# Kernel optimization log

Measured on AMD Instinct MI355X. Metric: run time of the kernel, lower is better.

## Reference

```python
import jax, jax.numpy as jnp
import numpy as np

B, S, DIM = 64, 256, 512
H = 16
DH = DIM // H          # 32
W = 256                # window_size == seq_len
ROPE_BASE = 10000.0


def _rope(x):
    # x: (B, S, H, DH), interleaved-pair RoPE
    pos = jnp.arange(S, dtype=jnp.float32)
    inv_freq = 1.0 / (ROPE_BASE ** (jnp.arange(0, DH, 2, dtype=jnp.float32) / DH))
    sinusoid = pos[:, None] * inv_freq[None, :]            # (S, DH/2)
    sin = jnp.sin(sinusoid)[None, :, None, :]              # (1, S, 1, DH/2)
    cos = jnp.cos(sinusoid)[None, :, None, :]
    x1 = x[..., 0::2]
    x2 = x[..., 1::2]
    r1 = x1 * cos - x2 * sin
    r2 = x1 * sin + x2 * cos
    return jnp.stack([r1, r2], axis=-1).reshape(x.shape)


def setup_inputs() -> dict:
    key = jax.random.key(0)
    ks = jax.random.split(key, 8)
    s = 1.0 / np.sqrt(DIM)
    return {
        "hidden_states": jax.random.normal(ks[0], (B, S, DIM), jnp.float32),
        "Wq": jax.random.normal(ks[1], (DIM, DIM), jnp.float32) * s,
        "bq": jnp.zeros((DIM,), jnp.float32),
        "Wk": jax.random.normal(ks[2], (DIM, DIM), jnp.float32) * s,
        "bk": jnp.zeros((DIM,), jnp.float32),
        "Wv": jax.random.normal(ks[3], (DIM, DIM), jnp.float32) * s,
        "bv": jnp.zeros((DIM,), jnp.float32),
        "bias_table": jax.random.normal(ks[4], (2 * W - 1, H), jnp.float32) * 0.02,
    }


def reference(hidden_states, Wq, bq, Wk, bk, Wv, bv, bias_table):
    b, s, _ = hidden_states.shape
    q = hidden_states @ Wq + bq
    k = hidden_states @ Wk + bk
    v = hidden_states @ Wv + bv
    # (B, S, H, DH)
    q = _rope(q.reshape(b, s, H, DH))
    k = _rope(k.reshape(b, s, H, DH))
    v = v.reshape(b, s, H, DH)
    # (B, H, S, DH)
    q = q.transpose(0, 2, 1, 3)
    k = k.transpose(0, 2, 1, 3)
    v = v.transpose(0, 2, 1, 3)
    scores = jnp.einsum('bhqd,bhkd->bhqk', q, k) / np.sqrt(DH)
    # relative_position_index[i, j] == (i - j) + W - 1
    rel_idx = jnp.arange(W)[:, None] - jnp.arange(W)[None, :] + (W - 1)
    rel_bias = bias_table[rel_idx]                 # (W, W, H)
    rel_bias = rel_bias.transpose(2, 0, 1)[None]   # (1, H, W, W)
    # NOTE: bias added AFTER softmax, faithful to the original module
    probs = jax.nn.softmax(scores, axis=-1) + rel_bias
    ctx = jnp.einsum('bhqk,bhkd->bhqd', probs, v)
    ctx = ctx.transpose(0, 2, 1, 3).reshape(b, s, DIM)
    return ctx
```

## Files before the change

kernel.cpp:

```cpp
#include <hip/hip_runtime.h>
#include <stdint.h>

typedef __attribute__((ext_vector_type(8))) short bf16x8;
typedef __attribute__((ext_vector_type(4))) float f32x4;
typedef __attribute__((ext_vector_type(4))) unsigned int u32x4;

#define MFMA16(a, b, c) __builtin_amdgcn_mfma_f32_16x16x32_bf16(a, b, c, 0, 0, 0)

__device__ __forceinline__ float bf2f(unsigned short u) {
    union { unsigned int i; float f; } x; x.i = ((unsigned int)u) << 16; return x.f;
}
__device__ __forceinline__ unsigned short f2bf(float f) {
    union { float f; unsigned int i; } x; x.f = f;
    unsigned int u = x.i;
    return (unsigned short)((u + 0x7FFFu + ((u >> 16) & 1u)) >> 16);
}

__global__ __launch_bounds__(256) void k_cvt(const float4* __restrict__ in,
                                             unsigned short* __restrict__ out) {
    int i = blockIdx.x * 256 + threadIdx.x;
    float4 v = in[i];
    ushort4 o;
    o.x = f2bf(v.x); o.y = f2bf(v.y); o.z = f2bf(v.z); o.w = f2bf(v.w);
    *(ushort4*)(out + (size_t)i * 4) = o;
}

__global__ __launch_bounds__(256) void k_wt(const float* __restrict__ W0,
                                            const float* __restrict__ W1,
                                            const float* __restrict__ W2,
                                            unsigned short* __restrict__ Wt) {
    __shared__ float t[64][65];
    const float* Wm = (blockIdx.z == 0) ? W0 : (blockIdx.z == 1) ? W1 : W2;
    int k0 = blockIdx.x * 64, n0 = blockIdx.y * 64;
    for (int it = 0; it < 16; ++it) {
        int idx = threadIdx.x + it * 256;
        int r = idx >> 6, c = idx & 63;
        t[r][c] = Wm[(k0 + r) * 512 + n0 + c];
    }
    __syncthreads();
    unsigned short* dst = Wt + (size_t)blockIdx.z * 512 * 512;
    for (int it = 0; it < 16; ++it) {
        int idx = threadIdx.x + it * 256;
        int nr = idx >> 6, kc = idx & 63;
        dst[(n0 + nr) * 512 + k0 + kc] = f2bf(t[kc][nr]);
    }
}

__global__ __launch_bounds__(256) void k_sc(float* __restrict__ cs2) {
    int s = threadIdx.x;
    for (int f = 0; f < 16; ++f) {
        float inv = powf(10000.0f, -(float)f / 16.0f);
        float a = (float)s * inv;
        cs2[(s * 16 + f) * 2 + 0] = cosf(a);
        cs2[(s * 16 + f) * 2 + 1] = sinf(a);
    }
}

__global__ __launch_bounds__(256, 2) void k_gemm(
    const unsigned short* __restrict__ A,
    const unsigned short* __restrict__ Bw,
    const float* __restrict__ bq, const float* __restrict__ bk, const float* __restrict__ bv,
    const float* __restrict__ cs2,
    unsigned short* __restrict__ Qo, unsigned short* __restrict__ Ko, unsigned short* __restrict__ Vo) {
    __shared__ unsigned short a_l[128 * 64];
    __shared__ unsigned short b_l[128 * 64];
    const int tid = threadIdx.x;
    const int wave = tid >> 6, lane = tid & 63;
    const int l15 = lane & 15, l4 = lane >> 4;
    int bid = blockIdx.x;
    int swz = (bid & 7) * 192 + (bid >> 3);
    const int m0 = (swz / 12) * 128;
    const int n0 = (swz % 12) * 128;
    const int wm = (wave >> 1) * 64, wn = (wave & 1) * 64;
    const bool isV = (n0 >= 1024);

    f32x4 zero4 = {0.f, 0.f, 0.f, 0.f};
    f32x4 acc[4][4];
#pragma unroll
    for (int i = 0; i < 4; ++i)
#pragma unroll
        for (int j = 0; j < 4; ++j) acc[i][j] = zero4;

    const int srow = tid >> 3;
    const int skc = (tid & 7) * 8;
    const unsigned short* ga = A + (size_t)(m0 + srow) * 512 + skc;
    const unsigned short* gb = Bw + (size_t)(n0 + srow) * 512 + skc;
    unsigned short* la = a_l + wave * 512;
    unsigned short* lb = b_l + wave * 512;

    for (int kt = 0; kt < 8; ++kt) {
        const unsigned short* pa = ga + kt * 64;
        const unsigned short* pb = gb + kt * 64;
#pragma unroll
        for (int it = 0; it < 4; ++it) {
            __builtin_amdgcn_global_load_lds(
                (const __attribute__((address_space(1))) unsigned int*)(pa + it * (32 * 512)),
                (__attribute__((address_space(3))) unsigned int*)(la + it * 2048), 16, 0, 0);
            __builtin_amdgcn_global_load_lds(
                (const __attribute__((address_space(1))) unsigned int*)(pb + it * (32 * 512)),
                (__attribute__((address_space(3))) unsigned int*)(lb + it * 2048), 16, 0, 0);
        }
        __syncthreads();
#pragma unroll
        for (int kc = 0; kc < 2; ++kc) {
            bf16x8 af[4], bfr[4];
#pragma unroll
            for (int i = 0; i < 4; ++i)
                af[i] = *(const bf16x8*)&a_l[(wm + i * 16 + l15) * 64 + kc * 32 + l4 * 8];
#pragma unroll
            for (int j = 0; j < 4; ++j)
                bfr[j] = *(const bf16x8*)&b_l[(wn + j * 16 + l15) * 64 + kc * 32 + l4 * 8];
            if (!isV) {
#pragma unroll
                for (int i = 0; i < 4; ++i)
#pragma unroll
                    for (int j = 0; j < 4; ++j) acc[i][j] = MFMA16(af[i], bfr[j], acc[i][j]);
            } else {
#pragma unroll
                for (int i = 0; i < 4; ++i)
#pragma unroll
                    for (int j = 0; j < 4; ++j) acc[i][j] = MFMA16(bfr[j], af[i], acc[i][j]);
            }
        }
        __syncthreads();
    }

    if (!isV) {
        const int mat = n0 >> 9;
        unsigned short* __restrict__ dst = (mat == 0) ? Qo : Ko;
        const float* __restrict__ bias = (mat == 0) ? bq : bk;
#pragma unroll
        for (int j = 0; j < 4; ++j) {
            int col = (n0 & 511) + wn + j * 16 + l15;
            float bb = bias[col];
            int h = col >> 5, dh = col & 31, f = dh >> 1;
            float sgn = (col & 1) ? 1.0f : -1.0f;
#pragma unroll
            for (int i = 0; i < 4; ++i) {
#pragma unroll
                for (int r = 0; r < 4; ++r) {
                    int m = m0 + wm + i * 16 + l4 * 4 + r;
                    int b = m >> 8, s = m & 255;
                    float t = acc[i][j][r] + bb;
                    float partner = __shfl_xor(t, 1);
                    float2 cn = *(const float2*)(cs2 + (s * 16 + f) * 2);
                    float o = t * cn.x + sgn * partner * cn.y;
                    dst[(size_t)(b * 16 + h) * 8192 + s * 32 + dh] = f2bf(o);
                }
            }
        }
    } else {
#pragma unroll
        for (int j = 0; j < 4; ++j) {
#pragma unroll
            for (int r = 0; r < 4; ++r) {
                int n = (n0 & 511) + wn + j * 16 + l4 * 4 + r;
                float bb = bv[n];
                int h = n >> 5, dh = n & 31;
#pragma unroll
                for (int i = 0; i < 4; ++i) {
                    int m = m0 + wm + i * 16 + l15;
                    int b = m >> 8, s = m & 255;
                    Vo[(size_t)(b * 16 + h) * 8192 + dh * 256 + s] = f2bf(acc[i][j][r] + bb);
                }
            }
        }
    }
}

__global__ __launch_bounds__(256, 2) void k_attn(
    const unsigned short* __restrict__ Qm, const unsigned short* __restrict__ Km,
    const unsigned short* __restrict__ Vm,
    const float* __restrict__ bias_table, float* __restrict__ out) {
    __shared__ unsigned short k_l[256 * 32];
    __shared__ unsigned short vt_l[32 * 256];
    __shared__ unsigned short p_l[64 * 264];
    __shared__ float bias_l[320];

    const int tid = threadIdx.x, wave = tid >> 6, lane = tid & 63;
    const int l15 = lane & 15, l4 = lane >> 4;
    int bid = blockIdx.x;
    int swz = (bid & 7) * 512 + (bid >> 3);
    const int qb = swz & 3, h = (swz >> 2) & 15, b = swz >> 6;
    const int q0 = qb * 64;
    const size_t bh = ((size_t)(b * 16 + h)) * 8192;

    for (int i = tid; i < 319; i += 256) bias_l[i] = bias_table[(q0 + i) * 16 + h];

#pragma unroll
    for (int it = 0; it < 4; ++it) {
        int p = it * 256 + wave * 64 + lane;
        __builtin_amdgcn_global_load_lds(
            (const __attribute__((address_space(1))) unsigned int*)(Km + bh + p * 8),
            (__attribute__((address_space(3))) unsigned int*)(k_l + it * 2048 + wave * 512), 16, 0, 0);
    }
#pragma unroll
    for (int it = 0; it < 4; ++it) {
        int p = it * 256 + wave * 64 + lane;
        int dh = p >> 5, cpos = p & 31;
        int srcc = cpos ^ (dh & 7);
        __builtin_amdgcn_global_load_lds(
            (const __attribute__((address_space(1))) unsigned int*)(Vm + bh + dh * 256 + srcc * 8),
            (__attribute__((address_space(3))) unsigned int*)(vt_l + it * 2048 + wave * 512), 16, 0, 0);
    }

    bf16x8 qfrag = *(const bf16x8*)(Qm + bh + (size_t)(q0 + 16 * wave + l15) * 32 + l4 * 8);
    __syncthreads();

    f32x4 zero4 = {0.f, 0.f, 0.f, 0.f};
    f32x4 sc[16];
#pragma unroll
    for (int ct = 0; ct < 16; ++ct) {
        bf16x8 kf = *(const bf16x8*)&k_l[(ct * 16 + l15) * 32 + l4 * 8];
        sc[ct] = MFMA16(kf, qfrag, zero4);
    }

    const float SCL2 = 0.17677669529663687f * 1.4426950408889634f;
    float sum = 0.f;
#pragma unroll
    for (int ct = 0; ct < 16; ++ct) {
#pragma unroll
        for (int r = 0; r < 4; ++r) {
            float e;
            float x = sc[ct][r] * SCL2;
            asm("v_exp_f32 %0, %1" : "=v"(e) : "v"(x));
            sc[ct][r] = e;
            sum += e;
        }
    }
    sum += __shfl_xor(sum, 16);
    sum += __shfl_xor(sum, 32);
    float inv = 1.0f / sum;

    const int qrow = 16 * wave + l15;
#pragma unroll
    for (int ct = 0; ct < 16; ++ct) {
        int kbase = 16 * ct + 4 * l4;
        int jb = qrow - kbase + 255;
        float p0 = sc[ct][0] * inv + bias_l[jb];
        float p1 = sc[ct][1] * inv + bias_l[jb - 1];
        float p2 = sc[ct][2] * inv + bias_l[jb - 2];
        float p3 = sc[ct][3] * inv + bias_l[jb - 3];
        uint2 w;
        w.x = (unsigned int)f2bf(p0) | ((unsigned int)f2bf(p1) << 16);
        w.y = (unsigned int)f2bf(p2) | ((unsigned int)f2bf(p3) << 16);
        *(uint2*)&p_l[qrow * 264 + kbase] = w;
    }

    f32x4 o0 = zero4, o1 = zero4;
#pragma unroll
    for (int kc = 0; kc < 8; ++kc) {
        bf16x8 pf = *(const bf16x8*)&p_l[qrow * 264 + kc * 32 + l4 * 8];
        int vc = (kc * 4 + l4) ^ (l15 & 7);
        bf16x8 v0 = *(const bf16x8*)&vt_l[l15 * 256 + vc * 8];
        bf16x8 v1 = *(const bf16x8*)&vt_l[(16 + l15) * 256 + vc * 8];
        o0 = MFMA16(pf, v0, o0);
        o1 = MFMA16(pf, v1, o1);
    }

#pragma unroll
    for (int r = 0; r < 4; ++r) {
        int s = q0 + 16 * wave + l4 * 4 + r;
        float* po = out + ((size_t)(b * 256 + s)) * 512 + h * 32;
        po[l15] = o0[r];
        po[16 + l15] = o1[r];
    }
}

extern "C" void kernel_launch(void* const* d_in, const int* in_sizes, int n_in,
                              void* d_out, int out_size, void* d_ws, size_t ws_size,
                              hipStream_t stream) {
    const float* hs = (const float*)d_in[0];
    const float* Wq = (const float*)d_in[1];
    const float* bq = (const float*)d_in[2];
    const float* Wk = (const float*)d_in[3];
    const float* bk = (const float*)d_in[4];
    const float* Wv = (const float*)d_in[5];
    const float* bv = (const float*)d_in[6];
    const float* bt = (const float*)d_in[7];
    float* out = (float*)d_out;

    char* ws = (char*)d_ws;
    unsigned short* hsb = (unsigned short*)ws;
    unsigned short* wt = (unsigned short*)(ws + 16777216);
    unsigned short* Qo = (unsigned short*)(ws + 18350080);
    unsigned short* Ko = (unsigned short*)(ws + 35127296);
    unsigned short* Vo = (unsigned short*)(ws + 51904512);
    float* cs2 = (float*)(ws + 68681728);

    hipLaunchKernelGGL(k_cvt, dim3(8192), dim3(256), 0, stream, (const float4*)hs, hsb);
    hipLaunchKernelGGL(k_wt, dim3(8, 8, 3), dim3(256), 0, stream, Wq, Wk, Wv, wt);
    hipLaunchKernelGGL(k_sc, dim3(1), dim3(256), 0, stream, cs2);
    hipLaunchKernelGGL(k_gemm, dim3(1536), dim3(256), 0, stream,
                       hsb, wt, bq, bk, bv, cs2, Qo, Ko, Vo);
    hipLaunchKernelGGL(k_attn, dim3(4096), dim3(256), 0, stream,
                       Qo, Ko, Vo, bt, out);
}
```

Measured before the change: 109.1 us.

## Double-buffer GEMM LDS tiles and XOR-swizzle the LDS layout

```diff
diff --git a/kernel.cpp b/kernel.cpp
--- a/kernel.cpp
+++ b/kernel.cpp
@@ -62,8 +62,8 @@
     const float* __restrict__ bq, const float* __restrict__ bk, const float* __restrict__ bv,
     const float* __restrict__ cs2,
     unsigned short* __restrict__ Qo, unsigned short* __restrict__ Ko, unsigned short* __restrict__ Vo) {
-    __shared__ unsigned short a_l[128 * 64];
-    __shared__ unsigned short b_l[128 * 64];
+    __shared__ unsigned short a_l[2][8192];
+    __shared__ unsigned short b_l[2][8192];
     const int tid = threadIdx.x;
     const int wave = tid >> 6, lane = tid & 63;
     const int l15 = lane & 15, l4 = lane >> 4;
@@ -82,48 +82,61 @@
         for (int j = 0; j < 4; ++j) acc[i][j] = zero4;
 
     const int srow = tid >> 3;
-    const int skc = (tid & 7) * 8;
+    const int skc = ((tid & 7) ^ (srow & 7)) * 8;
     const unsigned short* ga = A + (size_t)(m0 + srow) * 512 + skc;
     const unsigned short* gb = Bw + (size_t)(n0 + srow) * 512 + skc;
-    unsigned short* la = a_l + wave * 512;
-    unsigned short* lb = b_l + wave * 512;
-
+
+#define STAGE(buf, kt)                                                                          \
+    {                                                                                           \
+        const unsigned short* pa = ga + (kt) * 64;                                              \
+        const unsigned short* pb = gb + (kt) * 64;                                              \
+        unsigned short* la = &a_l[(buf)][wave * 512];                                           \
+        unsigned short* lb = &b_l[(buf)][wave * 512];                                           \
+        _Pragma("unroll")                                                                       \
+        for (int it = 0; it < 4; ++it) {                                                        \
+            __builtin_amdgcn_global_load_lds(                                                   \
+                (const __attribute__((address_space(1))) unsigned int*)(pa + it * (32 * 512)),  \
+                (__attribute__((address_space(3))) unsigned int*)(la + it * 2048), 16, 0, 0);   \
+            __builtin_amdgcn_global_load_lds(                                                   \
+                (const __attribute__((address_space(1))) unsigned int*)(pb + it * (32 * 512)),  \
+                (__attribute__((address_space(3))) unsigned int*)(lb + it * 2048), 16, 0, 0);   \
+        }                                                                                       \
+    }
+
+    STAGE(0, 0);
+    __syncthreads();
+    int cur = 0;
     for (int kt = 0; kt < 8; ++kt) {
-        const unsigned short* pa = ga + kt * 64;
-        const unsigned short* pb = gb + kt * 64;
-#pragma unroll
-        for (int it = 0; it < 4; ++it) {
-            __builtin_amdgcn_global_load_lds(
-                (const __attribute__((address_space(1))) unsigned int*)(pa + it * (32 * 512)),
-                (__attribute__((address_space(3))) unsigned int*)(la + it * 2048), 16, 0, 0);
-            __builtin_amdgcn_global_load_lds(
-                (const __attribute__((address_space(1))) unsigned int*)(pb + it * (32 * 512)),
-                (__attribute__((address_space(3))) unsigned int*)(lb + it * 2048), 16, 0, 0);
+        if (kt < 7) STAGE(cur ^ 1, kt + 1);
+#pragma unroll
+        for (int kc = 0; kc < 2; ++kc) {
+            bf16x8 af[4], bfr[4];
+#pragma unroll
+            for (int i = 0; i < 4; ++i) {
+                int g = ((kc * 4 + l4) ^ (l15 & 7)) * 8;
+                af[i] = *(const bf16x8*)&a_l[cur][(wm + i * 16 + l15) * 64 + g];
+            }
+#pragma unroll
+            for (int j = 0; j < 4; ++j) {
+                int g = ((kc * 4 + l4) ^ (l15 & 7)) * 8;
+                bfr[j] = *(const bf16x8*)&b_l[cur][(wn + j * 16 + l15) * 64 + g];
+            }
+            if (!isV) {
+#pragma unroll
+                for (int i = 0; i < 4; ++i)
+#pragma unroll
+                    for (int j = 0; j < 4; ++j) acc[i][j] = MFMA16(af[i], bfr[j], acc[i][j]);
+            } else {
+#pragma unroll
+                for (int i = 0; i < 4; ++i)
+#pragma unroll
+                    for (int j = 0; j < 4; ++j) acc[i][j] = MFMA16(bfr[j], af[i], acc[i][j]);
+            }
         }
         __syncthreads();
-#pragma unroll
-        for (int kc = 0; kc < 2; ++kc) {
-            bf16x8 af[4], bfr[4];
-#pragma unroll
-            for (int i = 0; i < 4; ++i)
-                af[i] = *(const bf16x8*)&a_l[(wm + i * 16 + l15) * 64 + kc * 32 + l4 * 8];
-#pragma unroll
-            for (int j = 0; j < 4; ++j)
-                bfr[j] = *(const bf16x8*)&b_l[(wn + j * 16 + l15) * 64 + kc * 32 + l4 * 8];
-            if (!isV) {
-#pragma unroll
-                for (int i = 0; i < 4; ++i)
-#pragma unroll
-                    for (int j = 0; j < 4; ++j) acc[i][j] = MFMA16(af[i], bfr[j], acc[i][j]);
-            } else {
-#pragma unroll
-                for (int i = 0; i < 4; ++i)
-#pragma unroll
-                    for (int j = 0; j < 4; ++j) acc[i][j] = MFMA16(bfr[j], af[i], acc[i][j]);
-            }
-        }
-        __syncthreads();
-    }
+        cur ^= 1;
+    }
+#undef STAGE
 
     if (!isV) {
         const int mat = n0 >> 9;
```

After: 98.38 us. 1.11x faster.
